# Kernel tuning notes

Measured on AMD Instinct MI355X. Metric: run time of the kernel, lower is better.

The kernel has to match this reference:

```python
import jax, jax.numpy as jnp
import numpy as np

IN, OUT, EDGE_FEAT = 32, 32, 16
B, N = 8, 128            # batch, nodes per graph; E = B*N*N edges
H1, H2, H3 = 128, 256, 128  # NNet hidden sizes (nmp_qc default)


def _linear_params(key, n_in, n_out):
    kw, kb = jax.random.split(key)
    s = 1.0 / np.sqrt(n_in)
    W = jax.random.uniform(kw, (n_in, n_out), jnp.float32, -s, s)
    b = jax.random.uniform(kb, (n_out,), jnp.float32, -s, s)
    return W, b


def setup_inputs() -> dict:
    key = jax.random.key(0)
    ks = jax.random.split(key, 8)
    h_v = jax.random.normal(ks[0], (B, N, IN), jnp.float32)
    h_w = jax.random.normal(ks[1], (B * N, IN), jnp.float32)
    e_vw = jax.random.normal(ks[2], (B * N * N, EDGE_FEAT), jnp.float32)
    W1, b1 = _linear_params(ks[3], EDGE_FEAT, H1)
    W2, b2 = _linear_params(ks[4], H1, H2)
    W3, b3 = _linear_params(ks[5], H2, H3)
    W4, b4 = _linear_params(ks[6], H3, IN * OUT)
    return {"h_v": h_v, "h_w": h_w, "e_vw": e_vw,
            "W1": W1, "b1": b1, "W2": W2, "b2": b2,
            "W3": W3, "b3": b3, "W4": W4, "b4": b4}


def reference(h_v, h_w, e_vw, W1, b1, W2, b2, W3, b3, W4, b4):
    # Edge-conditioned weight generator (NNet MLP with ReLU hidden layers)
    x = jax.nn.relu(e_vw @ W1 + b1)
    x = jax.nn.relu(x @ W2 + b2)
    x = jax.nn.relu(x @ W3 + b3)
    edge_output = x @ W4 + b4                      # (E, out*in)
    edge_output = edge_output.reshape(-1, OUT, IN)  # (E, out, in)

    # h_w_rows: expand h_w (B*N, in) with a trailing dim of size h_v.size(1)=N,
    # then flatten to rows of length `in` (exact replica of the torch view).
    n_v = h_v.shape[1]
    h_w_rows = jnp.broadcast_to(h_w[:, :, None],
                                (h_w.shape[0], h_w.shape[1], n_v))
    h_w_rows = h_w_rows.reshape(-1, IN)            # (E, in)

    # bmm of per-edge (out, in) matrix with (in,) vector, then squeeze
    m_new = jnp.einsum('eoi,ei->eo', edge_output, h_w_rows)  # (E, out)
    return m_new
```

## Files before the change

### kernel.cpp

```cpp
#include <hip/hip_runtime.h>


typedef _Float16 f16;
typedef _Float16 f16x8 __attribute__((ext_vector_type(8)));
typedef __fp16 fp16x2 __attribute__((ext_vector_type(2)));
typedef float f32x4 __attribute__((ext_vector_type(4)));

#define OFF_W1S 0
#define OFF_W2S 4096
#define OFF_W3S 36864
#define OFF_W4S 69632
#define WS_HALFS 73728

union U16x8 { struct { uint2 lo, hi; } p; f16x8 v; };
union U32x2 { fp16x2 h2[2]; uint2 u; };

__global__ void prep_kernel(const float* __restrict__ W1, const float* __restrict__ b1,
                            const float* __restrict__ W2, const float* __restrict__ W3,
                            const float* __restrict__ W4, const float* __restrict__ b4,
                            f16* __restrict__ wsh, float* __restrict__ b4r) {
  int t = blockIdx.x * 256 + threadIdx.x;
  if (t < 4096) {
    int j = t & 7, l = (t >> 3) & 63, ct = t >> 9;
    int k = ((l >> 4) & 3) * 8 + j, c = ct * 16 + (l & 15);
    wsh[OFF_W1S + t] = (k < 16) ? (f16)W1[k * 128 + c]
                                : (k == 16 ? (f16)b1[c] : (f16)0.f);
  } else if (t < 36864) {
    int s = t - 4096;
    int j = s & 7, l = (s >> 3) & 63, kt = (s >> 9) & 3, ct = s >> 11;
    int k = kt * 32 + ((l >> 4) & 3) * 8 + j, c = ct * 16 + (l & 15);
    wsh[t] = (f16)W2[k * 256 + c];
  } else if (t < 69632) {
    int s = t - 36864;
    int j = s & 7, l = (s >> 3) & 63, kt = (s >> 9) & 7, ct = s >> 12;
    int k = kt * 32 + ((l >> 4) & 3) * 8 + j, c = ct * 16 + (l & 15);
    wsh[t] = (f16)W3[k * 128 + c];
  } else if (t < 73728) {
    int s = t - 69632;
    int j = s & 7, l = (s >> 3) & 63, kt = (s >> 9) & 3, ct = s >> 11;
    int k = kt * 32 + ((l >> 4) & 3) * 8 + j, o = ct * 16 + (l & 15);
    float a = 0.f;
#pragma unroll
    for (int i = 0; i < 32; ++i) a += W4[k * 1024 + o * 32 + i];
    wsh[t] = (f16)a;
  }
  if (t < 32) {
    float a = 0.f;
#pragma unroll
    for (int i = 0; i < 32; ++i) a += b4[t * 32 + i];
    b4r[t] = a;
  }
}

__global__ __launch_bounds__(256, 3) void mlp_mfma_kernel(
    const float* __restrict__ e_vw, const float* __restrict__ h_w,
    const float* __restrict__ b2, const float* __restrict__ b3,
    const f16* __restrict__ wsh, const float* __restrict__ b4r,
    float* __restrict__ out) {
  __shared__ f16 P[64 * 132];
  __shared__ f16 Q[64 * 260];

  const int l  = threadIdx.x & 63;
  const int w  = threadIdx.x >> 6;
  const int e0 = l & 15;
  const int kg = l >> 4;
  const size_t row0 = (size_t)blockIdx.x * 64;

  const f16x8* wp1 = (const f16x8*)(wsh + OFF_W1S);
  const f16x8* wp2 = (const f16x8*)(wsh + OFF_W2S);
  const f16x8* wp3 = (const f16x8*)(wsh + OFF_W3S);
  const f16x8* wp4 = (const f16x8*)(wsh + OFF_W4S);

  {
    f16x8 bfr1[2];
#pragma unroll
    for (int c = 0; c < 2; ++c) bfr1[c] = wp1[(2 * w + c) * 64 + l];
#pragma unroll
    for (int t = 0; t < 4; ++t) {
      U16x8 a;
      if (kg < 2) {
        const float* pe = e_vw + (row0 + t * 16 + e0) * 16 + kg * 8;
        float4 v0 = *reinterpret_cast<const float4*>(pe);
        float4 v1 = *reinterpret_cast<const float4*>(pe + 4);
        U32x2 c0, c1;
        c0.h2[0] = __builtin_amdgcn_cvt_pkrtz(v0.x, v0.y);
        c0.h2[1] = __builtin_amdgcn_cvt_pkrtz(v0.z, v0.w);
        c1.h2[0] = __builtin_amdgcn_cvt_pkrtz(v1.x, v1.y);
        c1.h2[1] = __builtin_amdgcn_cvt_pkrtz(v1.z, v1.w);
        a.p.lo = c0.u; a.p.hi = c1.u;
      } else {
        a.p.lo.x = (kg == 2) ? 0x00003C00u : 0u;
        a.p.lo.y = 0u; a.p.hi.x = 0u; a.p.hi.y = 0u;
      }
#pragma unroll
      for (int c = 0; c < 2; ++c) {
        f32x4 acc = {0.f, 0.f, 0.f, 0.f};
        acc = __builtin_amdgcn_mfma_f32_16x16x32_f16(bfr1[c], a.v, acc, 0, 0, 0);
        U32x2 o;
        o.h2[0] = __builtin_amdgcn_cvt_pkrtz(fmaxf(acc[0], 0.f), fmaxf(acc[1], 0.f));
        o.h2[1] = __builtin_amdgcn_cvt_pkrtz(fmaxf(acc[2], 0.f), fmaxf(acc[3], 0.f));
        *reinterpret_cast<uint2*>(P + (t * 16 + e0) * 132 + (2 * w + c) * 16 + kg * 4) = o.u;
      }
    }
  }
  f16x8 bfr2[16];
#pragma unroll
  for (int c = 0; c < 4; ++c)
#pragma unroll
    for (int kt = 0; kt < 4; ++kt)
      bfr2[c * 4 + kt] = wp2[((4 * w + c) * 4 + kt) * 64 + l];
  __syncthreads();

  {
    float4 bb[4];
#pragma unroll
    for (int c = 0; c < 4; ++c)
      bb[c] = *reinterpret_cast<const float4*>(b2 + (4 * w + c) * 16 + kg * 4);
#pragma unroll
    for (int t = 0; t < 4; ++t) {
      const f16* pa = P + (t * 16 + e0) * 132 + kg * 8;
      U16x8 a[4];
#pragma unroll
      for (int kt = 0; kt < 4; ++kt) {
        a[kt].p.lo = *(const uint2*)(pa + kt * 32);
        a[kt].p.hi = *(const uint2*)(pa + kt * 32 + 4);
      }
#pragma unroll
      for (int c = 0; c < 4; ++c) {
        f32x4 acc = {0.f, 0.f, 0.f, 0.f};
#pragma unroll
        for (int kt = 0; kt < 4; ++kt)
          acc = __builtin_amdgcn_mfma_f32_16x16x32_f16(bfr2[c * 4 + kt], a[kt].v, acc, 0, 0, 0);
        U32x2 o;
        o.h2[0] = __builtin_amdgcn_cvt_pkrtz(fmaxf(acc[0] + bb[c].x, 0.f),
                                             fmaxf(acc[1] + bb[c].y, 0.f));
        o.h2[1] = __builtin_amdgcn_cvt_pkrtz(fmaxf(acc[2] + bb[c].z, 0.f),
                                             fmaxf(acc[3] + bb[c].w, 0.f));
        *reinterpret_cast<uint2*>(Q + (t * 16 + e0) * 260 + (4 * w + c) * 16 + kg * 4) = o.u;
      }
    }
  }
  f16x8 bfr3[16];
#pragma unroll
  for (int c = 0; c < 2; ++c)
#pragma unroll
    for (int kt = 0; kt < 8; ++kt)
      bfr3[c * 8 + kt] = wp3[((2 * w + c) * 8 + kt) * 64 + l];
  __syncthreads();

  {
    float4 bb[2];
#pragma unroll
    for (int c = 0; c < 2; ++c)
      bb[c] = *reinterpret_cast<const float4*>(b3 + (2 * w + c) * 16 + kg * 4);
#pragma unroll
    for (int t = 0; t < 4; ++t) {
      const f16* pa = Q + (t * 16 + e0) * 260 + kg * 8;
      U16x8 a[8];
#pragma unroll
      for (int kt = 0; kt < 8; ++kt) {
        a[kt].p.lo = *(const uint2*)(pa + kt * 32);
        a[kt].p.hi = *(const uint2*)(pa + kt * 32 + 4);
      }
#pragma unroll
      for (int c = 0; c < 2; ++c) {
        f32x4 acc = {0.f, 0.f, 0.f, 0.f};
#pragma unroll
        for (int kt = 0; kt < 8; ++kt)
          acc = __builtin_amdgcn_mfma_f32_16x16x32_f16(bfr3[c * 8 + kt], a[kt].v, acc, 0, 0, 0);
        U32x2 o;
        o.h2[0] = __builtin_amdgcn_cvt_pkrtz(fmaxf(acc[0] + bb[c].x, 0.f),
                                             fmaxf(acc[1] + bb[c].y, 0.f));
        o.h2[1] = __builtin_amdgcn_cvt_pkrtz(fmaxf(acc[2] + bb[c].z, 0.f),
                                             fmaxf(acc[3] + bb[c].w, 0.f));
        *reinterpret_cast<uint2*>(P + (t * 16 + e0) * 132 + (2 * w + c) * 16 + kg * 4) = o.u;
      }
    }
  }
  const int ct = w & 1;
  const int tb = (w >> 1) * 2;
  f16x8 bfr4[4];
#pragma unroll
  for (int kt = 0; kt < 4; ++kt) bfr4[kt] = wp4[(ct * 4 + kt) * 64 + l];
  __syncthreads();

  {
    float4 bb = *reinterpret_cast<const float4*>(b4r + ct * 16 + kg * 4);
#pragma unroll
    for (int ti = 0; ti < 2; ++ti) {
      int t = tb + ti;
      const f16* pa = P + (t * 16 + e0) * 132 + kg * 8;
      U16x8 a[4];
#pragma unroll
      for (int kt = 0; kt < 4; ++kt) {
        a[kt].p.lo = *(const uint2*)(pa + kt * 32);
        a[kt].p.hi = *(const uint2*)(pa + kt * 32 + 4);
      }
      f32x4 acc = {0.f, 0.f, 0.f, 0.f};
#pragma unroll
      for (int kt = 0; kt < 4; ++kt)
        acc = __builtin_amdgcn_mfma_f32_16x16x32_f16(bfr4[kt], a[kt].v, acc, 0, 0, 0);
      size_t e = row0 + t * 16 + e0;
      float s = h_w[(e >> 7) * 32 + ((e & 127) >> 2)];
      float4 st;
      st.x = s * (acc[0] + bb.x); st.y = s * (acc[1] + bb.y);
      st.z = s * (acc[2] + bb.z); st.w = s * (acc[3] + bb.w);
      *reinterpret_cast<float4*>(out + e * 32 + ct * 16 + kg * 4) = st;
    }
  }
}

extern "C" void kernel_launch(void* const* d_in, const int* in_sizes, int n_in,
                              void* d_out, int out_size, void* d_ws, size_t ws_size,
                              hipStream_t stream) {
  const float* h_w  = (const float*)d_in[1];
  const float* e_vw = (const float*)d_in[2];
  const float* W1   = (const float*)d_in[3];
  const float* b1   = (const float*)d_in[4];
  const float* W2   = (const float*)d_in[5];
  const float* b2   = (const float*)d_in[6];
  const float* W3   = (const float*)d_in[7];
  const float* b3   = (const float*)d_in[8];
  const float* W4   = (const float*)d_in[9];
  const float* b4   = (const float*)d_in[10];
  float* out = (float*)d_out;

  f16*   wsh = (f16*)d_ws;
  float* b4r = (float*)((char*)d_ws + (size_t)WS_HALFS * 2);

  const int E = in_sizes[2] / 16;

  hipLaunchKernelGGL(prep_kernel, dim3(288), dim3(256), 0, stream,
                     W1, b1, W2, W3, W4, b4, wsh, b4r);
  hipLaunchKernelGGL(mlp_mfma_kernel, dim3(E / 64), dim3(256), 0, stream,
                     e_vw, h_w, b2, b3, wsh, b4r, out);
}
```

Measured before the change: 33.22 us.

## Keep activations in registers and stage W2/W3 weights in shared memory

Restructures the fused MLP so each wave owns 32 edges and carries hidden activations between layers in registers. The weight layout is permuted so an MFMA output fragment can be reused directly as the next layer's input fragment, which removes the P/Q shared-memory round trips and all but one barrier. W2 and W3 (128 KB in fp16) are copied into shared memory once per 512-thread block, and blocks now cover 256 edges. The trade-off is much higher LDS use per block, which limits occupancy, plus more register pressure and repeated weight reads from LDS in every wave.

```diff
diff --git a/kernel.cpp b/kernel.cpp
--- a/kernel.cpp
+++ b/kernel.cpp
@@ -21,24 +21,27 @@
                             f16* __restrict__ wsh, float* __restrict__ b4r) {
   int t = blockIdx.x * 256 + threadIdx.x;
   if (t < 4096) {
-    int j = t & 7, l = (t >> 3) & 63, ct = t >> 9;
-    int k = ((l >> 4) & 3) * 8 + j, c = ct * 16 + (l & 15);
+    int j = t & 7, lq = (t >> 3) & 63, ct = t >> 9;
+    int k = ((lq >> 4) & 3) * 8 + j, c = ct * 16 + (lq & 15);
     wsh[OFF_W1S + t] = (k < 16) ? (f16)W1[k * 128 + c]
                                 : (k == 16 ? (f16)b1[c] : (f16)0.f);
   } else if (t < 36864) {
     int s = t - 4096;
-    int j = s & 7, l = (s >> 3) & 63, kt = (s >> 9) & 3, ct = s >> 11;
-    int k = kt * 32 + ((l >> 4) & 3) * 8 + j, c = ct * 16 + (l & 15);
+    int j = s & 7, lq = (s >> 3) & 63, kt = (s >> 9) & 3, ct = s >> 11;
+    int u = (lq >> 4) & 3;
+    int k = kt * 32 + (j >> 2) * 16 + u * 4 + (j & 3), c = ct * 16 + (lq & 15);
     wsh[t] = (f16)W2[k * 256 + c];
   } else if (t < 69632) {
     int s = t - 36864;
-    int j = s & 7, l = (s >> 3) & 63, kt = (s >> 9) & 7, ct = s >> 12;
-    int k = kt * 32 + ((l >> 4) & 3) * 8 + j, c = ct * 16 + (l & 15);
+    int j = s & 7, lq = (s >> 3) & 63, kt = (s >> 9) & 7, ct = s >> 12;
+    int u = (lq >> 4) & 3;
+    int k = kt * 32 + (j >> 2) * 16 + u * 4 + (j & 3), c = ct * 16 + (lq & 15);
     wsh[t] = (f16)W3[k * 128 + c];
   } else if (t < 73728) {
     int s = t - 69632;
-    int j = s & 7, l = (s >> 3) & 63, kt = (s >> 9) & 3, ct = s >> 11;
-    int k = kt * 32 + ((l >> 4) & 3) * 8 + j, o = ct * 16 + (l & 15);
+    int j = s & 7, lq = (s >> 3) & 63, kt = (s >> 9) & 3, ct = s >> 11;
+    int u = (lq >> 4) & 3;
+    int k = kt * 32 + (j >> 2) * 16 + u * 4 + (j & 3), o = ct * 16 + (lq & 15);
     float a = 0.f;
 #pragma unroll
     for (int i = 0; i < 32; ++i) a += W4[k * 1024 + o * 32 + i];
@@ -52,160 +55,123 @@
   }
 }
 
-__global__ __launch_bounds__(256, 3) void mlp_mfma_kernel(
+__device__ __forceinline__ uint2 relu_pack(f32x4 a) {
+  U32x2 o;
+  o.h2[0] = __builtin_amdgcn_cvt_pkrtz(fmaxf(a[0], 0.f), fmaxf(a[1], 0.f));
+  o.h2[1] = __builtin_amdgcn_cvt_pkrtz(fmaxf(a[2], 0.f), fmaxf(a[3], 0.f));
+  return o.u;
+}
+__device__ __forceinline__ uint2 bias_relu_pack(f32x4 a, float4 b) {
+  U32x2 o;
+  o.h2[0] = __builtin_amdgcn_cvt_pkrtz(fmaxf(a[0] + b.x, 0.f), fmaxf(a[1] + b.y, 0.f));
+  o.h2[1] = __builtin_amdgcn_cvt_pkrtz(fmaxf(a[2] + b.z, 0.f), fmaxf(a[3] + b.w, 0.f));
+  return o.u;
+}
+
+__global__ __launch_bounds__(512, 2) void mlp_mfma_kernel(
     const float* __restrict__ e_vw, const float* __restrict__ h_w,
     const float* __restrict__ b2, const float* __restrict__ b3,
     const f16* __restrict__ wsh, const float* __restrict__ b4r,
     float* __restrict__ out) {
-  __shared__ f16 P[64 * 132];
-  __shared__ f16 Q[64 * 260];
-
-  const int l  = threadIdx.x & 63;
-  const int w  = threadIdx.x >> 6;
-  const int e0 = l & 15;
-  const int kg = l >> 4;
-  const size_t row0 = (size_t)blockIdx.x * 64;
+  __shared__ f16 WT[65536];
+
+  const int tid = threadIdx.x;
+  const int l = tid & 63, w = tid >> 6;
+  const int e0 = l & 15, u = l >> 4;
+  const size_t base = (size_t)blockIdx.x * 256 + (size_t)w * 32;
 
   const f16x8* wp1 = (const f16x8*)(wsh + OFF_W1S);
-  const f16x8* wp2 = (const f16x8*)(wsh + OFF_W2S);
-  const f16x8* wp3 = (const f16x8*)(wsh + OFF_W3S);
   const f16x8* wp4 = (const f16x8*)(wsh + OFF_W4S);
 
+  U16x8 xin[2];
+#pragma unroll
+  for (int ti = 0; ti < 2; ++ti) {
+    if (u < 2) {
+      const float* pe = e_vw + (base + ti * 16 + e0) * 16 + u * 8;
+      float4 v0 = *reinterpret_cast<const float4*>(pe);
+      float4 v1 = *reinterpret_cast<const float4*>(pe + 4);
+      U32x2 c0, c1;
+      c0.h2[0] = __builtin_amdgcn_cvt_pkrtz(v0.x, v0.y);
+      c0.h2[1] = __builtin_amdgcn_cvt_pkrtz(v0.z, v0.w);
+      c1.h2[0] = __builtin_amdgcn_cvt_pkrtz(v1.x, v1.y);
+      c1.h2[1] = __builtin_amdgcn_cvt_pkrtz(v1.z, v1.w);
+      xin[ti].p.lo = c0.u; xin[ti].p.hi = c1.u;
+    } else {
+      xin[ti].p.lo.x = (u == 2) ? 0x00003C00u : 0u;
+      xin[ti].p.lo.y = 0u; xin[ti].p.hi.x = 0u; xin[ti].p.hi.y = 0u;
+    }
+  }
+  f16x8 w1f[8];
+#pragma unroll
+  for (int ct = 0; ct < 8; ++ct) w1f[ct] = wp1[ct * 64 + l];
+
   {
-    f16x8 bfr1[2];
-#pragma unroll
-    for (int c = 0; c < 2; ++c) bfr1[c] = wp1[(2 * w + c) * 64 + l];
-#pragma unroll
-    for (int t = 0; t < 4; ++t) {
-      U16x8 a;
-      if (kg < 2) {
-        const float* pe = e_vw + (row0 + t * 16 + e0) * 16 + kg * 8;
-        float4 v0 = *reinterpret_cast<const float4*>(pe);
-        float4 v1 = *reinterpret_cast<const float4*>(pe + 4);
-        U32x2 c0, c1;
-        c0.h2[0] = __builtin_amdgcn_cvt_pkrtz(v0.x, v0.y);
-        c0.h2[1] = __builtin_amdgcn_cvt_pkrtz(v0.z, v0.w);
-        c1.h2[0] = __builtin_amdgcn_cvt_pkrtz(v1.x, v1.y);
-        c1.h2[1] = __builtin_amdgcn_cvt_pkrtz(v1.z, v1.w);
-        a.p.lo = c0.u; a.p.hi = c1.u;
-      } else {
-        a.p.lo.x = (kg == 2) ? 0x00003C00u : 0u;
-        a.p.lo.y = 0u; a.p.hi.x = 0u; a.p.hi.y = 0u;
-      }
-#pragma unroll
-      for (int c = 0; c < 2; ++c) {
-        f32x4 acc = {0.f, 0.f, 0.f, 0.f};
-        acc = __builtin_amdgcn_mfma_f32_16x16x32_f16(bfr1[c], a.v, acc, 0, 0, 0);
-        U32x2 o;
-        o.h2[0] = __builtin_amdgcn_cvt_pkrtz(fmaxf(acc[0], 0.f), fmaxf(acc[1], 0.f));
-        o.h2[1] = __builtin_amdgcn_cvt_pkrtz(fmaxf(acc[2], 0.f), fmaxf(acc[3], 0.f));
-        *reinterpret_cast<uint2*>(P + (t * 16 + e0) * 132 + (2 * w + c) * 16 + kg * 4) = o.u;
-      }
-    }
-  }
-  f16x8 bfr2[16];
-#pragma unroll
-  for (int c = 0; c < 4; ++c)
-#pragma unroll
-    for (int kt = 0; kt < 4; ++kt)
-      bfr2[c * 4 + kt] = wp2[((4 * w + c) * 4 + kt) * 64 + l];
+    const float4* src = (const float4*)(wsh + OFF_W2S);
+    float4* dst = (float4*)WT;
+#pragma unroll
+    for (int i = 0; i < 16; ++i) dst[tid + i * 512] = src[tid + i * 512];
+  }
   __syncthreads();
 
-  {
-    float4 bb[4];
-#pragma unroll
-    for (int c = 0; c < 4; ++c)
-      bb[c] = *reinterpret_cast<const float4*>(b2 + (4 * w + c) * 16 + kg * 4);
-#pragma unroll
-    for (int t = 0; t < 4; ++t) {
-      const f16* pa = P + (t * 16 + e0) * 132 + kg * 8;
-      U16x8 a[4];
-#pragma unroll
-      for (int kt = 0; kt < 4; ++kt) {
-        a[kt].p.lo = *(const uint2*)(pa + kt * 32);
-        a[kt].p.hi = *(const uint2*)(pa + kt * 32 + 4);
-      }
-#pragma unroll
-      for (int c = 0; c < 4; ++c) {
-        f32x4 acc = {0.f, 0.f, 0.f, 0.f};
-#pragma unroll
-        for (int kt = 0; kt < 4; ++kt)
-          acc = __builtin_amdgcn_mfma_f32_16x16x32_f16(bfr2[c * 4 + kt], a[kt].v, acc, 0, 0, 0);
-        U32x2 o;
-        o.h2[0] = __builtin_amdgcn_cvt_pkrtz(fmaxf(acc[0] + bb[c].x, 0.f),
-                                             fmaxf(acc[1] + bb[c].y, 0.f));
-        o.h2[1] = __builtin_amdgcn_cvt_pkrtz(fmaxf(acc[2] + bb[c].z, 0.f),
-                                             fmaxf(acc[3] + bb[c].w, 0.f));
-        *reinterpret_cast<uint2*>(Q + (t * 16 + e0) * 260 + (4 * w + c) * 16 + kg * 4) = o.u;
-      }
-    }
-  }
-  f16x8 bfr3[16];
-#pragma unroll
-  for (int c = 0; c < 2; ++c)
-#pragma unroll
-    for (int kt = 0; kt < 8; ++kt)
-      bfr3[c * 8 + kt] = wp3[((2 * w + c) * 8 + kt) * 64 + l];
-  __syncthreads();
-
-  {
-    float4 bb[2];
-#pragma unroll
-    for (int c = 0; c < 2; ++c)
-      bb[c] = *reinterpret_cast<const float4*>(b3 + (2 * w + c) * 16 + kg * 4);
-#pragma unroll
-    for (int t = 0; t < 4; ++t) {
-      const f16* pa = Q + (t * 16 + e0) * 260 + kg * 8;
-      U16x8 a[8];
-#pragma unroll
-      for (int kt = 0; kt < 8; ++kt) {
-        a[kt].p.lo = *(const uint2*)(pa + kt * 32);
-        a[kt].p.hi = *(const uint2*)(pa + kt * 32 + 4);
-      }
-#pragma unroll
-      for (int c = 0; c < 2; ++c) {
-        f32x4 acc = {0.f, 0.f, 0.f, 0.f};
-#pragma unroll
-        for (int kt = 0; kt < 8; ++kt)
-          acc = __builtin_amdgcn_mfma_f32_16x16x32_f16(bfr3[c * 8 + kt], a[kt].v, acc, 0, 0, 0);
-        U32x2 o;
-        o.h2[0] = __builtin_amdgcn_cvt_pkrtz(fmaxf(acc[0] + bb[c].x, 0.f),
-                                             fmaxf(acc[1] + bb[c].y, 0.f));
-        o.h2[1] = __builtin_amdgcn_cvt_pkrtz(fmaxf(acc[2] + bb[c].z, 0.f),
-                                             fmaxf(acc[3] + bb[c].w, 0.f));
-        *reinterpret_cast<uint2*>(P + (t * 16 + e0) * 132 + (2 * w + c) * 16 + kg * 4) = o.u;
-      }
-    }
-  }
-  const int ct = w & 1;
-  const int tb = (w >> 1) * 2;
-  f16x8 bfr4[4];
-#pragma unroll
-  for (int kt = 0; kt < 4; ++kt) bfr4[kt] = wp4[(ct * 4 + kt) * 64 + l];
-  __syncthreads();
-
-  {
-    float4 bb = *reinterpret_cast<const float4*>(b4r + ct * 16 + kg * 4);
-#pragma unroll
-    for (int ti = 0; ti < 2; ++ti) {
-      int t = tb + ti;
-      const f16* pa = P + (t * 16 + e0) * 132 + kg * 8;
-      U16x8 a[4];
-#pragma unroll
-      for (int kt = 0; kt < 4; ++kt) {
-        a[kt].p.lo = *(const uint2*)(pa + kt * 32);
-        a[kt].p.hi = *(const uint2*)(pa + kt * 32 + 4);
-      }
-      f32x4 acc = {0.f, 0.f, 0.f, 0.f};
+  U16x8 x1[2][4];
+  const f32x4 z4 = {0.f, 0.f, 0.f, 0.f};
+#pragma unroll
+  for (int ct = 0; ct < 8; ++ct) {
+    f32x4 a0 = __builtin_amdgcn_mfma_f32_16x16x32_f16(w1f[ct], xin[0].v, z4, 0, 0, 0);
+    f32x4 a1 = __builtin_amdgcn_mfma_f32_16x16x32_f16(w1f[ct], xin[1].v, z4, 0, 0, 0);
+    uint2 d0 = relu_pack(a0), d1 = relu_pack(a1);
+    if (ct & 1) { x1[0][ct >> 1].p.hi = d0; x1[1][ct >> 1].p.hi = d1; }
+    else        { x1[0][ct >> 1].p.lo = d0; x1[1][ct >> 1].p.lo = d1; }
+  }
+
+  U16x8 x2[2][8];
+#pragma unroll
+  for (int ct = 0; ct < 16; ++ct) {
+    f32x4 a0 = z4, a1 = z4;
+#pragma unroll
+    for (int kt = 0; kt < 4; ++kt) {
+      f16x8 wf = *(const f16x8*)(WT + ((ct * 4 + kt) * 64 + l) * 8);
+      a0 = __builtin_amdgcn_mfma_f32_16x16x32_f16(wf, x1[0][kt].v, a0, 0, 0, 0);
+      a1 = __builtin_amdgcn_mfma_f32_16x16x32_f16(wf, x1[1][kt].v, a1, 0, 0, 0);
+    }
+    float4 bb = *reinterpret_cast<const float4*>(b2 + ct * 16 + u * 4);
+    uint2 d0 = bias_relu_pack(a0, bb), d1 = bias_relu_pack(a1, bb);
+    if (ct & 1) { x2[0][ct >> 1].p.hi = d0; x2[1][ct >> 1].p.hi = d1; }
+    else        { x2[0][ct >> 1].p.lo = d0; x2[1][ct >> 1].p.lo = d1; }
+  }
+
+  U16x8 x3[2][4];
+#pragma unroll
+  for (int ct = 0; ct < 8; ++ct) {
+    f32x4 a0 = z4, a1 = z4;
+#pragma unroll
+    for (int kt = 0; kt < 8; ++kt) {
+      f16x8 wf = *(const f16x8*)(WT + 32768 + ((ct * 8 + kt) * 64 + l) * 8);
+      a0 = __builtin_amdgcn_mfma_f32_16x16x32_f16(wf, x2[0][kt].v, a0, 0, 0, 0);
+      a1 = __builtin_amdgcn_mfma_f32_16x16x32_f16(wf, x2[1][kt].v, a1, 0, 0, 0);
+    }
+    float4 bb = *reinterpret_cast<const float4*>(b3 + ct * 16 + u * 4);
+    uint2 d0 = bias_relu_pack(a0, bb), d1 = bias_relu_pack(a1, bb);
+    if (ct & 1) { x3[0][ct >> 1].p.hi = d0; x3[1][ct >> 1].p.hi = d1; }
+    else        { x3[0][ct >> 1].p.lo = d0; x3[1][ct >> 1].p.lo = d1; }
+  }
+
+#pragma unroll
+  for (int ti = 0; ti < 2; ++ti) {
+    size_t e = base + ti * 16 + e0;
+    float s = h_w[(e >> 7) * 32 + ((e & 127) >> 2)];
+#pragma unroll
+    for (int ct = 0; ct < 2; ++ct) {
+      f32x4 acc = z4;
 #pragma unroll
       for (int kt = 0; kt < 4; ++kt)
-        acc = __builtin_amdgcn_mfma_f32_16x16x32_f16(bfr4[kt], a[kt].v, acc, 0, 0, 0);
-      size_t e = row0 + t * 16 + e0;
-      float s = h_w[(e >> 7) * 32 + ((e & 127) >> 2)];
+        acc = __builtin_amdgcn_mfma_f32_16x16x32_f16(wp4[(ct * 4 + kt) * 64 + l],
+                                                     x3[ti][kt].v, acc, 0, 0, 0);
+      float4 bb = *reinterpret_cast<const float4*>(b4r + ct * 16 + u * 4);
       float4 st;
       st.x = s * (acc[0] + bb.x); st.y = s * (acc[1] + bb.y);
       st.z = s * (acc[2] + bb.z); st.w = s * (acc[3] + bb.w);
-      *reinterpret_cast<float4*>(out + e * 32 + ct * 16 + kg * 4) = st;
+      *reinterpret_cast<float4*>(out + e * 32 + ct * 16 + u * 4) = st;
     }
   }
 }
@@ -229,9 +195,10 @@
   float* b4r = (float*)((char*)d_ws + (size_t)WS_HALFS * 2);
 
   const int E = in_sizes[2] / 16;
+  const int blocks = E / 256;
 
   hipLaunchKernelGGL(prep_kernel, dim3(288), dim3(256), 0, stream,
                      W1, b1, W2, W3, W4, b4, wsh, b4r);
-  hipLaunchKernelGGL(mlp_mfma_kernel, dim3(E / 64), dim3(256), 0, stream,
+  hipLaunchKernelGGL(mlp_mfma_kernel, dim3(blocks), dim3(512), 0, stream,
                      e_vw, h_w, b2, b3, wsh, b4r, out);
 }
```

Result: faster. 30.03 us (-9.6%).
